# Kernel tuning notes

Measured on AMD Instinct MI355X. Metric: run time of the kernel, lower is better.

The kernel has to match this reference:

```python
import jax, jax.numpy as jnp
import numpy as np

EPS = 1e-12  # F.normalize default eps


def build_graph(src, tgt):
    # src,tgt: (b, wh, c). torch does this under no_grad -> stop_gradient.
    logits = jnp.einsum('bnc,bmc->bnm', src, tgt)      # (b, wh, wh)
    g = jax.nn.softmax(logits, axis=-1)                # row softmax
    g = g / jnp.clip(jnp.sum(jnp.abs(g), axis=-2, keepdims=True), EPS)  # L1 norm over dim=-2
    return jax.lax.stop_gradient(g)


def gconv(A, source, message, Wa, ba, Wu, bu):
    # Gconv (PCA-GM style): A @ relu(Linear_a(message)) + relu(Linear_u(source))
    ax = jax.nn.relu(jnp.einsum('bnc,cd->bnd', message, Wa) + ba)
    ux = jax.nn.relu(jnp.einsum('bnc,cd->bnd', source, Wu) + bu)
    return jnp.einsum('bnm,bmd->bnd', A, ax) + ux


def setup_inputs() -> dict:
    key = jax.random.key(0)
    ks = jax.random.split(key, 10)
    b, c, h, w = 4, 256, 64, 64
    scale = 1.0 / np.sqrt(c)
    inp = {
        'skt': jax.random.normal(ks[0], (b, c, h, w), jnp.float32),
        'ref': jax.random.normal(ks[1], (b, c, h, w), jnp.float32),
        'Wa3': jax.random.normal(ks[2], (c, c), jnp.float32) * scale,
        'ba3': jnp.zeros((c,), jnp.float32),
        'Wu3': jax.random.normal(ks[3], (c, c), jnp.float32) * scale,
        'bu3': jnp.zeros((c,), jnp.float32),
        'Wa4': jax.random.normal(ks[4], (c, c), jnp.float32) * scale,
        'ba4': jnp.zeros((c,), jnp.float32),
        'Wu4': jax.random.normal(ks[5], (c, c), jnp.float32) * scale,
        'bu4': jnp.zeros((c,), jnp.float32),
    }
    return inp


def reference(skt, ref, Wa3, ba3, Wu3, bu3, Wa4, ba4, Wu4, bu4):
    b, c, h, w = skt.shape
    skt_f = skt.reshape(b, c, h * w).transpose(0, 2, 1)  # (b, wh, c)
    ref_f = ref.reshape(b, c, h * w).transpose(0, 2, 1)
    sr = build_graph(skt_f, ref_f)                       # (b, wh, wh)
    gen = gconv(sr, skt_f, ref_f, Wa3, ba3, Wu3, bu3) + skt_f
    gg = build_graph(gen, gen)
    ggen = gconv(gg, gen, gen, Wa4, ba4, Wu4, bu4) + gen
    return ggen
```

## Files before the change

### kernel.cpp

```cpp
#include <hip/hip_runtime.h>
#include <cstdint>
#include <cstddef>

#define WH 4096
#define CD 256
typedef long long i64;

typedef __attribute__((ext_vector_type(8))) _Float16 f16x8;
typedef __attribute__((ext_vector_type(4))) float f32x4;

#define AS1 __attribute__((address_space(1)))
#define AS3 __attribute__((address_space(3)))

__device__ __forceinline__ unsigned short f2h(float f) {
    _Float16 h = (_Float16)f;
    return __builtin_bit_cast(unsigned short, h);
}
__device__ __forceinline__ float h2f(unsigned short u) {
    return (float)__builtin_bit_cast(_Float16, u);
}
__device__ __forceinline__ void ld16_lds(const void* g, void* l) {
    __builtin_amdgcn_global_load_lds((AS1 void*)g, (AS3 void*)l, 16, 0, 0);
}

struct TransArgs {
    const float* src[8];
    unsigned short* dhi[8];
    unsigned short* dlo[8];
};
__global__ __launch_bounds__(256) void k_transN(TransArgs ta, int RR, int CC) {
    __shared__ float t[32][33];
    const float* s = ta.src[blockIdx.z];
    unsigned short* dhi = ta.dhi[blockIdx.z];
    unsigned short* dlo = ta.dlo[blockIdx.z];
    const int c0 = blockIdx.x * 32, r0 = blockIdx.y * 32;
    const int tx = threadIdx.x, ty = threadIdx.y;
#pragma unroll
    for (int i = 0; i < 4; ++i)
        t[ty + i * 8][tx] = s[(i64)(r0 + ty + i * 8) * CC + c0 + tx];
    __syncthreads();
#pragma unroll
    for (int i = 0; i < 4; ++i) {
        const i64 idx = (i64)(c0 + ty + i * 8) * RR + r0 + tx;
        const float v = t[tx][ty + i * 8];
        const unsigned short hi = f2h(v);
        dhi[idx] = hi;
        dlo[idx] = f2h(v - h2f(hi));
    }
}

template <int SPLIT3>
__global__ __launch_bounds__(256) void k_gemm12(
    const unsigned short* __restrict__ Shi, const unsigned short* __restrict__ Slo,
    const unsigned short* __restrict__ Mhi, const unsigned short* __restrict__ Mlo,
    const unsigned short* __restrict__ WAh, const unsigned short* __restrict__ WAl,
    const unsigned short* __restrict__ WUh, const unsigned short* __restrict__ WUl,
    const float* __restrict__ ba, const float* __restrict__ bu,
    unsigned short* __restrict__ axh, unsigned short* __restrict__ axl,
    float* __restrict__ outf) {
    __shared__ __align__(16) short lA[SPLIT3 ? 8192 : 4096];
    __shared__ __align__(16) short lB[SPLIT3 ? 8192 : 4096];
    const int mode = blockIdx.z >> 2;
    const int zb = blockIdx.z & 3;
    const i64 WHC = (i64)WH * CD;
    const unsigned short* A  = (mode ? Shi : Mhi) + (i64)zb * WHC;
    const unsigned short* A2 = SPLIT3 ? ((mode ? Slo : Mlo) + (i64)zb * WHC) : nullptr;
    const unsigned short* B  = mode ? WUh : WAh;
    const unsigned short* B2 = SPLIT3 ? (mode ? WUl : WAl) : nullptr;
    const float* bias = mode ? bu : ba;

    const int tid = threadIdx.x;
    const int w = tid >> 6, l = tid & 63;
    const int wm = w >> 1, wn = w & 1;
    const int bm = blockIdx.y * 128, bn = blockIdx.x * 128;
    const int l15 = l & 15, lq = l >> 4;

    f32x4 acc[4][4] = {};

    for (int kt = 0; kt < CD; kt += 32) {
        __syncthreads();
#pragma unroll
        for (int rr = 0; rr < 2; ++rr) {
            const int r = w + rr * 4;
            const int kb = r >> 1, mh = r & 1;
            const int row = mh * 64 + l;
            const i64 ao = (i64)(bm + row) * CD + kt + kb * 8;
            const i64 bo = (i64)(bn + row) * CD + kt + kb * 8;
            ld16_lds(A + ao, (char*)lA + r * 1024);
            ld16_lds(B + bo, (char*)lB + r * 1024);
            if constexpr (SPLIT3) {
                ld16_lds(A2 + ao, (char*)lA + 8192 + r * 1024);
                ld16_lds(B2 + bo, (char*)lB + 8192 + r * 1024);
            }
        }
        __syncthreads();
        f16x8 ah[4], bh[4], al[4], bl[4];
#pragma unroll
        for (int i = 0; i < 4; ++i) {
            const int ia = (lq * 128 + wm * 64 + i * 16 + l15) * 8;
            const int ib = (lq * 128 + wn * 64 + i * 16 + l15) * 8;
            ah[i] = *(const f16x8*)(lA + ia);
            bh[i] = *(const f16x8*)(lB + ib);
            if constexpr (SPLIT3) {
                al[i] = *(const f16x8*)(lA + 4096 + ia);
                bl[i] = *(const f16x8*)(lB + 4096 + ib);
            }
        }
#pragma unroll
        for (int i = 0; i < 4; ++i)
#pragma unroll
            for (int j = 0; j < 4; ++j) {
                acc[i][j] = __builtin_amdgcn_mfma_f32_16x16x32_f16(ah[i], bh[j], acc[i][j], 0, 0, 0);
                if constexpr (SPLIT3) {
                    acc[i][j] = __builtin_amdgcn_mfma_f32_16x16x32_f16(ah[i], bl[j], acc[i][j], 0, 0, 0);
                    acc[i][j] = __builtin_amdgcn_mfma_f32_16x16x32_f16(al[i], bh[j], acc[i][j], 0, 0, 0);
                }
            }
    }

#pragma unroll
    for (int i = 0; i < 4; ++i)
#pragma unroll
        for (int j = 0; j < 4; ++j) {
            const int n = bn + wn * 64 + j * 16 + l15;
            const int m0 = bm + wm * 64 + i * 16 + lq * 4;
            const float bv = bias[n];
            if (mode == 0) {
                unsigned short hv[4], lv[4];
#pragma unroll
                for (int r = 0; r < 4; ++r) {
                    const float v = fmaxf(acc[i][j][r] + bv, 0.f);
                    hv[r] = f2h(v);
                    lv[r] = f2h(v - h2f(hv[r]));
                }
                const i64 tb = (i64)zb * WHC + (i64)n * WH + m0;
                *(ushort4*)(axh + tb) = make_ushort4(hv[0], hv[1], hv[2], hv[3]);
                *(ushort4*)(axl + tb) = make_ushort4(lv[0], lv[1], lv[2], lv[3]);
            } else {
#pragma unroll
                for (int r = 0; r < 4; ++r) {
                    const i64 idx = (i64)zb * WHC + (i64)(m0 + r) * CD + n;
                    float v = fmaxf(acc[i][j][r] + bv, 0.f);
                    v += h2f(Shi[idx]) + h2f(Slo[idx]);
                    outf[idx] = v;
                }
            }
        }
}

__global__ __launch_bounds__(256, 2) void k_logits(
    const unsigned short* __restrict__ A, const unsigned short* __restrict__ A2,
    const unsigned short* __restrict__ B, const unsigned short* __restrict__ B2,
    unsigned short* __restrict__ G, float2* __restrict__ rowP, i64 sAB) {
    __shared__ __align__(16) short lA[16384];
    __shared__ __align__(16) short lB[8192];
    const int z = blockIdx.z;
    A += (i64)z * sAB; A2 += (i64)z * sAB;
    B += (i64)z * sAB; B2 += (i64)z * sAB;
    G += (i64)z * ((i64)WH * WH);
    rowP += (i64)z * (64 * (i64)WH);
    const int tid = threadIdx.x;
    const int w = tid >> 6, l = tid & 63;
    const int wm = w >> 1, wn = w & 1;
    const int bm = blockIdx.y * 256, bn = blockIdx.x * 128;
    const int l15 = l & 15, lq = l >> 4;

    f32x4 acc[8][4] = {};

    for (int kt = 0; kt < CD; kt += 32) {
        __syncthreads();
#pragma unroll
        for (int rr = 0; rr < 12; ++rr) {
            const int r = w + rr * 4;
            if (r < 32) {
                const int ra = r & 15;
                const int kb = ra >> 2, nh = ra & 3;
                const i64 ao = (i64)(bm + nh * 64 + l) * CD + kt + kb * 8;
                if (r < 16) ld16_lds(A + ao, (char*)lA + ra * 1024);
                else        ld16_lds(A2 + ao, (char*)lA + 16384 + ra * 1024);
            } else {
                const int rb = r & 7;
                const int kb = rb >> 1, mh = rb & 1;
                const i64 bo = (i64)(bn + mh * 64 + l) * CD + kt + kb * 8;
                if (r < 40) ld16_lds(B + bo, (char*)lB + rb * 1024);
                else        ld16_lds(B2 + bo, (char*)lB + 8192 + rb * 1024);
            }
        }
        __syncthreads();
        f16x8 bh[4], bl[4];
#pragma unroll
        for (int j = 0; j < 4; ++j) {
            const int ib = (lq * 128 + wn * 64 + j * 16 + l15) * 8;
            bh[j] = *(const f16x8*)(lB + ib);
            bl[j] = *(const f16x8*)(lB + 4096 + ib);
        }
#pragma unroll
        for (int i = 0; i < 8; ++i) {
            const int ia = (lq * 256 + wm * 128 + i * 16 + l15) * 8;
            const f16x8 ah = *(const f16x8*)(lA + ia);
            const f16x8 al = *(const f16x8*)(lA + 8192 + ia);
#pragma unroll
            for (int j = 0; j < 4; ++j) {
                acc[i][j] = __builtin_amdgcn_mfma_f32_16x16x32_f16(ah, bh[j], acc[i][j], 0, 0, 0);
                acc[i][j] = __builtin_amdgcn_mfma_f32_16x16x32_f16(ah, bl[j], acc[i][j], 0, 0, 0);
                acc[i][j] = __builtin_amdgcn_mfma_f32_16x16x32_f16(al, bh[j], acc[i][j], 0, 0, 0);
            }
        }
    }

#pragma unroll
    for (int i = 0; i < 8; ++i)
#pragma unroll
        for (int r = 0; r < 4; ++r) {
            const int grow = bm + wm * 128 + i * 16 + lq * 4 + r;
            float m = fmaxf(fmaxf(acc[i][0][r], acc[i][1][r]), fmaxf(acc[i][2][r], acc[i][3][r]));
            m = fmaxf(m, __shfl_xor(m, 1));
            m = fmaxf(m, __shfl_xor(m, 2));
            m = fmaxf(m, __shfl_xor(m, 4));
            m = fmaxf(m, __shfl_xor(m, 8));
            float s = 0.f;
#pragma unroll
            for (int j = 0; j < 4; ++j) {
                const float es = __expf((acc[i][j][r] - m) * 0.5f);
                s += es * es;
                G[(i64)grow * WH + bn + wn * 64 + j * 16 + l15] = f2h(es * 256.f);
            }
            s += __shfl_xor(s, 1); s += __shfl_xor(s, 2);
            s += __shfl_xor(s, 4); s += __shfl_xor(s, 8);
            if (l15 == 0)
                rowP[(i64)(blockIdx.x * 2 + wn) * WH + grow] = make_float2(m, s);
        }
}

__global__ __launch_bounds__(256) void k_colpart(const unsigned short* __restrict__ G,
                                                 const float2* __restrict__ rowP,
                                                 float* __restrict__ o,
                                                 float* __restrict__ part) {
    __shared__ float os[64];
    __shared__ float fl[4][64];
    const int z = blockIdx.z;
    G += (i64)z * ((i64)WH * WH);
    rowP += (i64)z * (64 * (i64)WH);
    o += (i64)z * WH;
    part += (i64)z * (64 * (i64)WH);
    const int t = threadIdx.x;
    const int r0 = blockIdx.y * 64;
    if (t < 64) {
        float M = -3.4e38f, S = 0.f;
        for (int x = 0; x < 64; ++x) {
            const float2 p = rowP[(i64)x * WH + r0 + t];
            const float nm = fmaxf(M, p.x);
            S = S * __expf(M - nm) + p.y * __expf(p.x - nm);
            M = nm;
        }
        const float ov = M + __logf(S);
        os[t] = ov;
        if (blockIdx.x == 0) o[r0 + t] = ov;
    }
    __syncthreads();
    {
        const int jt = t & 3, r = t >> 2;
        fl[jt][r] = __expf(rowP[(i64)(blockIdx.x * 4 + jt) * WH + r0 + r].x - os[r])
                  * (1.f / 65536.f);
    }
    __syncthreads();
    const int j = blockIdx.x * 256 + t;
    const int jt = t >> 6;
    float ps = 0.f;
#pragma unroll 4
    for (int r = 0; r < 64; ++r) {
        const float gv = h2f(G[(i64)(r0 + r) * WH + j]);
        ps += gv * gv * fl[jt][r];
    }
    part[(i64)blockIdx.y * WH + j] = ps;
}

template <int FULL>
__global__ __launch_bounds__(256) void k_attn(
    const unsigned short* __restrict__ G, const float* __restrict__ o,
    const float2* __restrict__ rowP, const float* __restrict__ part,
    const unsigned short* __restrict__ Bh, const unsigned short* __restrict__ Bl,
    unsigned short* __restrict__ Pw) {
    __shared__ __align__(16) short lL[4096];
    __shared__ __align__(16) short lBh[4096];
    __shared__ __align__(16) short lBl[FULL ? 4096 : 8];
    __shared__ float lS[512];
    const int zb = blockIdx.z >> 3;
    const int zc = blockIdx.z & 7;
    G += (i64)zb * ((i64)WH * WH);
    o += (i64)zb * WH;
    rowP += (i64)zb * (64 * (i64)WH);
    part += (i64)zb * (64 * (i64)WH);
    Bh += (i64)zb * ((i64)WH * CD);
    if constexpr (FULL) Bl += (i64)zb * ((i64)WH * CD);
    Pw += (i64)zb * (8 * (i64)WH * CD);
    const int tid = threadIdx.x;
    const int w = tid >> 6, l = tid & 63;
    const int wm = w >> 1, wn = w & 1;
    const int bm = blockIdx.y * 128, bn = blockIdx.x * 128;
    const int l15 = l & 15, lq = l >> 4;
    const i64 koff = (i64)zc * 512;

    {
        float C0 = 0.f, C1 = 0.f;
#pragma unroll 4
        for (int p = 0; p < 64; ++p) {
            C0 += part[(i64)p * WH + koff + tid];
            C1 += part[(i64)p * WH + koff + 256 + tid];
        }
        lS[tid] = 1.f / fmaxf(C0, 1e-12f);
        lS[tid + 256] = 1.f / fmaxf(C1, 1e-12f);
    }
    float o4[4];
#pragma unroll
    for (int i = 0; i < 4; ++i) o4[i] = o[bm + wm * 64 + i * 16 + l15];

    float fi[4];
    f32x4 acc[4][4] = {};
    for (int kt = 0; kt < 512; kt += 32) {
        __syncthreads();
#pragma unroll
        for (int rr = 0; rr < 2; ++rr) {
            const int r = w + rr * 4;
            const int kb = r >> 1, mh = r & 1;
            ld16_lds(G + (i64)(bm + mh * 64 + l) * WH + koff + kt + kb * 8,
                     (char*)lL + r * 1024);
        }
#pragma unroll
        for (int rr = 0; rr < 2; ++rr) {
            const int r = w + rr * 4;
            const int kb = r >> 1, mh = r & 1;
            const i64 bo = (i64)(bn + mh * 64 + l) * WH + koff + kt + kb * 8;
            ld16_lds(Bh + bo, (char*)lBh + r * 1024);
            if constexpr (FULL) ld16_lds(Bl + bo, (char*)lBl + r * 1024);
        }
        if ((kt & 32) == 0) {
            const i64 half = (koff + kt) >> 6;
#pragma unroll
            for (int i = 0; i < 4; ++i)
                fi[i] = __expf(rowP[half * WH + bm + wm * 64 + i * 16 + l15].x - o4[i])
                      * (1.f / 65536.f);
        }
        __syncthreads();
        float sv[8];
        *(float4*)(sv)     = *(const float4*)(lS + kt + lq * 8);
        *(float4*)(sv + 4) = *(const float4*)(lS + kt + lq * 8 + 4);
        f16x8 bh[4], bl[4];
#pragma unroll
        for (int j = 0; j < 4; ++j) {
            const int ib = (lq * 128 + wn * 64 + j * 16 + l15) * 8;
            bh[j] = *(const f16x8*)(lBh + ib);
            if constexpr (FULL) bl[j] = *(const f16x8*)(lBl + ib);
        }
#pragma unroll
        for (int i = 0; i < 4; ++i) {
            const f16x8 graw = *(const f16x8*)(lL + (lq * 128 + wm * 64 + i * 16 + l15) * 8);
            const float fi_ = fi[i];
            f16x8 ah, al;
#pragma unroll
            for (int e = 0; e < 8; ++e) {
                const float gv = (float)graw[e];
                const float a = gv * gv * fi_ * sv[e];
                const _Float16 hh = (_Float16)a;
                ah[e] = hh;
                if constexpr (FULL) al[e] = (_Float16)(a - (float)hh);
            }
#pragma unroll
            for (int j = 0; j < 4; ++j) {
                acc[i][j] = __builtin_amdgcn_mfma_f32_16x16x32_f16(ah, bh[j], acc[i][j], 0, 0, 0);
                if constexpr (FULL) {
                    acc[i][j] = __builtin_amdgcn_mfma_f32_16x16x32_f16(ah, bl[j], acc[i][j], 0, 0, 0);
                    acc[i][j] = __builtin_amdgcn_mfma_f32_16x16x32_f16(al, bh[j], acc[i][j], 0, 0, 0);
                }
            }
        }
    }
    unsigned short* P = Pw + (i64)zc * ((i64)WH * CD);
#pragma unroll
    for (int i = 0; i < 4; ++i)
#pragma unroll
        for (int j = 0; j < 4; ++j) {
            const int n = bn + wn * 64 + j * 16 + l15;
            const int m0 = bm + wm * 64 + i * 16 + lq * 4;
#pragma unroll
            for (int r = 0; r < 4; ++r)
                P[(i64)(m0 + r) * CD + n] = f2h(acc[i][j][r]);
        }
}

template <int SPLIT>
__global__ __launch_bounds__(256) void k_red(const unsigned short* __restrict__ Pw,
                                             float* __restrict__ outp,
                                             unsigned short* __restrict__ hi,
                                             unsigned short* __restrict__ lo) {
    const int b = blockIdx.y;
    Pw += (i64)b * (8 * (i64)WH * CD);
    outp += (i64)b * ((i64)WH * CD);
    if constexpr (SPLIT) {
        hi += (i64)b * ((i64)WH * CD);
        lo += (i64)b * ((i64)WH * CD);
    }
    const i64 i = ((i64)blockIdx.x * 256 + threadIdx.x) * 4;
    float4 a = *(const float4*)(outp + i);
#pragma unroll
    for (int z = 0; z < 8; ++z) {
        const ushort4 p = *(const ushort4*)(Pw + (i64)z * ((i64)WH * CD) + i);
        a.x += h2f(p.x); a.y += h2f(p.y); a.z += h2f(p.z); a.w += h2f(p.w);
    }
    *(float4*)(outp + i) = a;
    if constexpr (SPLIT) {
        ushort4 h, l2;
        h.x = f2h(a.x); l2.x = f2h(a.x - h2f(h.x));
        h.y = f2h(a.y); l2.y = f2h(a.y - h2f(h.y));
        h.z = f2h(a.z); l2.z = f2h(a.z - h2f(h.z));
        h.w = f2h(a.w); l2.w = f2h(a.w - h2f(h.w));
        *(ushort4*)(hi + i) = h;
        *(ushort4*)(lo + i) = l2;
    }
}

extern "C" void kernel_launch(void* const* d_in, const int* in_sizes, int n_in,
                              void* d_out, int out_size, void* d_ws, size_t ws_size,
                              hipStream_t stream) {
    (void)in_sizes; (void)n_in; (void)out_size; (void)ws_size;
    const float* skt = (const float*)d_in[0];
    const float* ref = (const float*)d_in[1];
    const float* Wa3 = (const float*)d_in[2];
    const float* ba3 = (const float*)d_in[3];
    const float* Wu3 = (const float*)d_in[4];
    const float* bu3 = (const float*)d_in[5];
    const float* Wa4 = (const float*)d_in[6];
    const float* ba4 = (const float*)d_in[7];
    const float* Wu4 = (const float*)d_in[8];
    const float* bu4 = (const float*)d_in[9];
    float* out = (float*)d_out;

    const i64 WHC = (i64)WH * CD;
    const i64 GM  = (i64)WH * WH;
    const i64 CC  = (i64)CD * CD;

    auto al = [](size_t x) { return (x + 255) & ~(size_t)255; };
    char* p = (char*)d_ws; size_t off = 0;
    auto carve = [&](size_t bytes) { void* r = p + off; off += al(bytes); return r; };
    unsigned short* Gb    = (unsigned short*)carve((size_t)2 * GM * 2);
    unsigned short* skthi = (unsigned short*)carve((size_t)4 * WHC * 2);
    unsigned short* sktlo = (unsigned short*)carve((size_t)4 * WHC * 2);
    unsigned short* refhi = (unsigned short*)carve((size_t)4 * WHC * 2);
    unsigned short* reflo = (unsigned short*)carve((size_t)4 * WHC * 2);
    unsigned short* ghi   = (unsigned short*)carve((size_t)4 * WHC * 2);
    unsigned short* glo   = (unsigned short*)carve((size_t)4 * WHC * 2);
    unsigned short* axthi = (unsigned short*)carve((size_t)4 * WHC * 2);
    unsigned short* axtlo = (unsigned short*)carve((size_t)4 * WHC * 2);
    float* ob             = (float*)carve((size_t)2 * WH * 4);
    float* partb          = (float*)carve((size_t)2 * 64 * WH * 4);
    float2* rowPb         = (float2*)carve((size_t)2 * 64 * WH * 8);
    unsigned short* Wthi  = (unsigned short*)carve((size_t)4 * CC * 2);
    unsigned short* Wtlo  = (unsigned short*)carve((size_t)4 * CC * 2);
    unsigned short* Pw    = (unsigned short*)carve((size_t)2 * 8 * WHC * 2);

    dim3 thr(256), ttr(32, 8);
    {
        TransArgs ta{};
        for (int b = 0; b < 4; ++b) {
            ta.src[b] = skt + (i64)b * WHC;     ta.src[b + 4] = ref + (i64)b * WHC;
            ta.dhi[b] = skthi + (i64)b * WHC;   ta.dhi[b + 4] = refhi + (i64)b * WHC;
            ta.dlo[b] = sktlo + (i64)b * WHC;   ta.dlo[b + 4] = reflo + (i64)b * WHC;
        }
        k_transN<<<dim3(WH / 32, CD / 32, 8), ttr, 0, stream>>>(ta, CD, WH);
        TransArgs tw{};
        const float* ws[4] = { Wa3, Wu3, Wa4, Wu4 };
        for (int i = 0; i < 4; ++i) {
            tw.src[i] = ws[i];
            tw.dhi[i] = Wthi + (i64)i * CC;
            tw.dlo[i] = Wtlo + (i64)i * CC;
        }
        k_transN<<<dim3(CD / 32, CD / 32, 4), ttr, 0, stream>>>(tw, CD, CD);
    }

    auto stage = [&](const unsigned short* shi, const unsigned short* slo,
                     const unsigned short* mhi, const unsigned short* mlo,
                     int widx, const float* ba, const float* bu, float* outf,
                     unsigned short* ohi, unsigned short* olo, int FULL3) {
        if (FULL3)
            k_gemm12<1><<<dim3(CD / 128, WH / 128, 8), thr, 0, stream>>>(
                shi, slo, mhi, mlo,
                Wthi + (i64)widx * CC, Wtlo + (i64)widx * CC,
                Wthi + (i64)(widx + 1) * CC, Wtlo + (i64)(widx + 1) * CC,
                ba, bu, axthi, axtlo, outf);
        else
            k_gemm12<0><<<dim3(CD / 128, WH / 128, 8), thr, 0, stream>>>(
                shi, slo, mhi, mlo,
                Wthi + (i64)widx * CC, nullptr,
                Wthi + (i64)(widx + 1) * CC, nullptr,
                ba, bu, axthi, axtlo, outf);
        for (int pb = 0; pb < 2; ++pb) {
            const i64 bo = (i64)(2 * pb) * WHC;
            k_logits<<<dim3(WH / 128, WH / 256, 2), thr, 0, stream>>>(
                shi + bo, slo + bo, mhi + bo, mlo + bo, Gb, rowPb, WHC);
            k_colpart<<<dim3(WH / 256, WH / 64, 2), thr, 0, stream>>>(Gb, rowPb, ob, partb);
            if (FULL3)
                k_attn<1><<<dim3(CD / 128, WH / 128, 16), thr, 0, stream>>>(
                    Gb, ob, rowPb, partb, axthi + bo, axtlo + bo, Pw);
            else
                k_attn<0><<<dim3(CD / 128, WH / 128, 16), thr, 0, stream>>>(
                    Gb, ob, rowPb, partb, axthi + bo, nullptr, Pw);
            if (ohi)
                k_red<1><<<dim3((unsigned)(WHC / 1024), 2), thr, 0, stream>>>(
                    Pw, outf + bo, ohi + bo, olo + bo);
            else
                k_red<0><<<dim3((unsigned)(WHC / 1024), 2), thr, 0, stream>>>(
                    Pw, outf + bo, nullptr, nullptr);
        }
    };

    stage(skthi, sktlo, refhi, reflo, 0, ba3, bu3, out, ghi, glo, 1);
    stage(ghi, glo, ghi, glo, 2, ba4, bu4, out, nullptr, nullptr, 0);
}
```

Before: 933.8 us.

## Widen attention tile to cover full channel dim, removing duplicate G loads

The attention GEMM block now covers all 256 output channels instead of 128, so each G tile and its squared, scaled A fragments are loaded and converted once rather than twice across the channel blocks. The grid drops the channel dimension, the LDS buffers for the B operand double, the accumulators double to 4x8 per wave, and B fragments are read from LDS inside the MFMA loop. This halves the block count and raises register and LDS pressure, which is hinted to the compiler with a launch-bounds minimum of 2 blocks.

```diff
diff --git a/kernel.cpp b/kernel.cpp
--- a/kernel.cpp
+++ b/kernel.cpp
@@ -276,17 +276,17 @@
 }
 
 template <int FULL>
-__global__ __launch_bounds__(256) void k_attn(
+__global__ __launch_bounds__(256, 2) void k_attn(
     const unsigned short* __restrict__ G, const float* __restrict__ o,
     const float2* __restrict__ rowP, const float* __restrict__ part,
     const unsigned short* __restrict__ Bh, const unsigned short* __restrict__ Bl,
     unsigned short* __restrict__ Pw) {
     __shared__ __align__(16) short lL[4096];
-    __shared__ __align__(16) short lBh[4096];
-    __shared__ __align__(16) short lBl[FULL ? 4096 : 8];
+    __shared__ __align__(16) short lBh[8192];
+    __shared__ __align__(16) short lBl[FULL ? 8192 : 8];
     __shared__ float lS[512];
-    const int zb = blockIdx.z >> 3;
-    const int zc = blockIdx.z & 7;
+    const int zb = blockIdx.y >> 3;
+    const int zc = blockIdx.y & 7;
     G += (i64)zb * ((i64)WH * WH);
     o += (i64)zb * WH;
     rowP += (i64)zb * (64 * (i64)WH);
@@ -297,7 +297,7 @@
     const int tid = threadIdx.x;
     const int w = tid >> 6, l = tid & 63;
     const int wm = w >> 1, wn = w & 1;
-    const int bm = blockIdx.y * 128, bn = blockIdx.x * 128;
+    const int bm = blockIdx.x * 128;
     const int l15 = l & 15, lq = l >> 4;
     const i64 koff = (i64)zc * 512;
 
@@ -316,7 +316,7 @@
     for (int i = 0; i < 4; ++i) o4[i] = o[bm + wm * 64 + i * 16 + l15];
 
     float fi[4];
-    f32x4 acc[4][4] = {};
+    f32x4 acc[4][8] = {};
     for (int kt = 0; kt < 512; kt += 32) {
         __syncthreads();
 #pragma unroll
@@ -327,10 +327,10 @@
                      (char*)lL + r * 1024);
         }
 #pragma unroll
-        for (int rr = 0; rr < 2; ++rr) {
+        for (int rr = 0; rr < 4; ++rr) {
             const int r = w + rr * 4;
-            const int kb = r >> 1, mh = r & 1;
-            const i64 bo = (i64)(bn + mh * 64 + l) * WH + koff + kt + kb * 8;
+            const int kb = r >> 2, rh = r & 3;
+            const i64 bo = (i64)(rh * 64 + l) * WH + koff + kt + kb * 8;
             ld16_lds(Bh + bo, (char*)lBh + r * 1024);
             if constexpr (FULL) ld16_lds(Bl + bo, (char*)lBl + r * 1024);
         }
@@ -345,13 +345,6 @@
         float sv[8];
         *(float4*)(sv)     = *(const float4*)(lS + kt + lq * 8);
         *(float4*)(sv + 4) = *(const float4*)(lS + kt + lq * 8 + 4);
-        f16x8 bh[4], bl[4];
-#pragma unroll
-        for (int j = 0; j < 4; ++j) {
-            const int ib = (lq * 128 + wn * 64 + j * 16 + l15) * 8;
-            bh[j] = *(const f16x8*)(lBh + ib);
-            if constexpr (FULL) bl[j] = *(const f16x8*)(lBl + ib);
-        }
 #pragma unroll
         for (int i = 0; i < 4; ++i) {
             const f16x8 graw = *(const f16x8*)(lL + (lq * 128 + wm * 64 + i * 16 + l15) * 8);
@@ -366,11 +359,14 @@
                 if constexpr (FULL) al[e] = (_Float16)(a - (float)hh);
             }
 #pragma unroll
-            for (int j = 0; j < 4; ++j) {
-                acc[i][j] = __builtin_amdgcn_mfma_f32_16x16x32_f16(ah, bh[j], acc[i][j], 0, 0, 0);
+            for (int j = 0; j < 8; ++j) {
+                const int ib = (lq * 256 + wn * 128 + j * 16 + l15) * 8;
+                const f16x8 bh = *(const f16x8*)(lBh + ib);
+                acc[i][j] = __builtin_amdgcn_mfma_f32_16x16x32_f16(ah, bh, acc[i][j], 0, 0, 0);
                 if constexpr (FULL) {
-                    acc[i][j] = __builtin_amdgcn_mfma_f32_16x16x32_f16(ah, bl[j], acc[i][j], 0, 0, 0);
-                    acc[i][j] = __builtin_amdgcn_mfma_f32_16x16x32_f16(al, bh[j], acc[i][j], 0, 0, 0);
+                    const f16x8 bl = *(const f16x8*)(lBl + ib);
+                    acc[i][j] = __builtin_amdgcn_mfma_f32_16x16x32_f16(ah, bl, acc[i][j], 0, 0, 0);
+                    acc[i][j] = __builtin_amdgcn_mfma_f32_16x16x32_f16(al, bh, acc[i][j], 0, 0, 0);
                 }
             }
         }
@@ -379,8 +375,8 @@
 #pragma unroll
     for (int i = 0; i < 4; ++i)
 #pragma unroll
-        for (int j = 0; j < 4; ++j) {
-            const int n = bn + wn * 64 + j * 16 + l15;
+        for (int j = 0; j < 8; ++j) {
+            const int n = wn * 128 + j * 16 + l15;
             const int m0 = bm + wm * 64 + i * 16 + lq * 4;
 #pragma unroll
             for (int r = 0; r < 4; ++r)
@@ -499,10 +495,10 @@
                 shi + bo, slo + bo, mhi + bo, mlo + bo, Gb, rowPb, WHC);
             k_colpart<<<dim3(WH / 256, WH / 64, 2), thr, 0, stream>>>(Gb, rowPb, ob, partb);
             if (FULL3)
-                k_attn<1><<<dim3(CD / 128, WH / 128, 16), thr, 0, stream>>>(
+                k_attn<1><<<dim3(WH / 128, 16), thr, 0, stream>>>(
                     Gb, ob, rowPb, partb, axthi + bo, axtlo + bo, Pw);
             else
-                k_attn<0><<<dim3(CD / 128, WH / 128, 16), thr, 0, stream>>>(
+                k_attn<0><<<dim3(WH / 128, 16), thr, 0, stream>>>(
                     Gb, ob, rowPb, partb, axthi + bo, nullptr, Pw);
             if (ohi)
                 k_red<1><<<dim3((unsigned)(WHC / 1024), 2), thr, 0, stream>>>(
```

After: 909.3 us. 2.6% less time.
